# Kernel optimization log

Measured on AMD Instinct MI355X. Metric: run time of the kernel, lower is better.

## Reference

```python
import jax, jax.numpy as jnp
import numpy as np

T, B, E, H = 64, 64, 128, 256
N_ITEMS, N_DATA = 50000, 20000
EPS = 1e-8


def setup_inputs() -> dict:
    key = jax.random.key(0)
    ks = jax.random.split(key, 20)
    lengths = jnp.sort(jax.random.randint(ks[0], (B,), 1, T + 1))[::-1]
    lengths = lengths.at[0].set(T)  # pack_padded_sequence expects max length first
    x = jax.random.randint(ks[1], (T, B), 1, N_ITEMS)
    tmask = jnp.arange(T)[:, None] < lengths[None, :]
    x = jnp.where(tmask, x, 0)  # padding index 0
    s = 0.05
    emb_table = (jax.random.normal(ks[2], (N_ITEMS, E)) * s).at[0].set(0.0)  # padding_idx=0
    data_embeddings = jax.random.normal(ks[3], (N_DATA, E)) * s
    return {
        'x': x, 'lengths': lengths,
        'emb_table': emb_table, 'data_embeddings': data_embeddings,
        'W_ih': jax.random.normal(ks[4], (4 * H, E)) * s,
        'W_hh': jax.random.normal(ks[5], (4 * H, H)) * s,
        'b_ih': jax.random.normal(ks[6], (4 * H,)) * s,
        'b_hh': jax.random.normal(ks[7], (4 * H,)) * s,
        'Wq': jax.random.normal(ks[8], (H, H)) * s, 'bq': jax.random.normal(ks[9], (H,)) * s,
        'Wk': jax.random.normal(ks[10], (H, H)) * s, 'bk': jax.random.normal(ks[11], (H,)) * s,
        'Wv': jax.random.normal(ks[12], (H, H)) * s, 'bv': jax.random.normal(ks[13], (H,)) * s,
        'W_out': jax.random.normal(ks[14], (E, H)) * s, 'b_out': jax.random.normal(ks[15], (E,)) * s,
    }


def _forward(x, lengths, emb_table, data_embeddings, W_ih, W_hh, b_ih, b_hh,
             Wq, bq, Wk, bk, Wv, bv, W_out, b_out):
    t_len, b_sz = x.shape
    e_dim = emb_table.shape[1]
    h_dim = W_hh.shape[1]

    embs0 = emb_table[x]  # (T, B, E); dropout is identity in eval mode
    initial_embs = jax.lax.stop_gradient(embs0)  # .clone().detach() in original

    # PositionalEncoding: original slices by x.size(1) == batch dim (faithful quirk)
    pos = jnp.arange(b_sz, dtype=jnp.float32)[:, None]
    div = jnp.exp(jnp.arange(0, e_dim, 2, dtype=jnp.float32) * (-jnp.log(10000.0) / e_dim))
    enc = jnp.stack([jnp.sin(pos * div), jnp.cos(pos * div)], axis=-1).reshape(b_sz, e_dim)
    embs = embs0 + enc[None, :, :]  # broadcast over time

    # single-layer LSTM over time (gate order i, f, g, o)
    def step(carry, x_t):
        h, c = carry
        gates = x_t @ W_ih.T + h @ W_hh.T + (b_ih + b_hh)  # (B, 4H)
        i, f, g, o = jnp.split(gates, 4, axis=-1)
        c = jax.nn.sigmoid(f) * c + jax.nn.sigmoid(i) * jnp.tanh(g)
        h = jax.nn.sigmoid(o) * jnp.tanh(c)
        return (h, c), h

    h0 = jnp.zeros((b_sz, h_dim), embs.dtype)
    (_, _), lstm_out = jax.lax.scan(step, (h0, h0), embs)  # (T, B, H)

    # pack/pad round-trip zeroes outputs past each length (LSTM is causal)
    tmask = jnp.arange(t_len)[:, None] < lengths[None, :]  # (T, B)
    lstm_out = lstm_out * tmask[:, :, None]
    lstm_out = lstm_out.transpose(1, 0, 2)  # (B, T, H)

    padding_mask = jnp.sum(lstm_out, axis=-1) != 0  # (B, T)

    q = lstm_out @ Wq.T + bq
    k = lstm_out @ Wk.T + bk
    v = lstm_out @ Wv.T + bv
    score = jnp.einsum('bth,bsh->bts', q, k) / jnp.sqrt(jnp.float32(h_dim))
    score = jnp.where(padding_mask[:, None, :], score, -jnp.inf)
    attn = jax.nn.softmax(score, axis=2)
    weighted = jnp.einsum('bts,bsh->bth', attn, v)  # (B, T, H)
    attn_output = jnp.mean(weighted, axis=1) @ W_out.T + b_out  # (B, E)

    # kNN: fused normalize + matmul + argmin + gather over all T at once
    qn = initial_embs / jnp.clip(jnp.linalg.norm(initial_embs, axis=-1, keepdims=True), EPS)
    dn = data_embeddings / jnp.clip(jnp.linalg.norm(data_embeddings, axis=-1, keepdims=True), EPS)
    sims = jnp.einsum('tbe,ne->tbn', qn, dn)  # (T, B, N_DATA)
    idx = jnp.argmax(sims, axis=-1)  # argmin of (1 - sim)
    closest = jnp.mean(data_embeddings[idx], axis=0)  # (B, E)

    attn_output = attn_output * closest
    return attn_output @ emb_table.T  # (B, n_items)


def reference(x, lengths, emb_table, data_embeddings, W_ih, W_hh, b_ih, b_hh,
              Wq, bq, Wk, bk, Wv, bv, W_out, b_out):
    return _forward(x, lengths, emb_table, data_embeddings, W_ih, W_hh, b_ih, b_hh,
                    Wq, bq, Wk, bk, Wv, bv, W_out, b_out)
```

## Files before the change

kernel.cpp:

```cpp
#include <hip/hip_runtime.h>

typedef unsigned int uint;
typedef unsigned short ushort;
typedef unsigned long long u64;

#define NITEMS 50000
#define NDATA  20000
#define BLKCAP 4096u
#define OVCAP  65536u

#define OFF_LSTMOUT   0x0000000ULL
#define OFF_HX        0x0400000ULL
#define OFF_HXM       0x0440000ULL
#define OFF_PACKED    0x0480000ULL
#define OFF_PACKED2   0x0488000ULL
#define OFF_HITCNTS   0x0490000ULL
#define OFF_OHITCNT   0x0490800ULL
#define MEMSET_BYTES  0x0491000ULL
#define OFF_QMARGIN   0x0491000ULL
#define OFF_XW        0x05A0000ULL
#define OFF_QKV       0x15A0000ULL
#define OFF_HITBUF    OFF_QKV
#define OFF_WIHT      0x21A0000ULL
#define OFF_WQKVT     0x2220000ULL
#define OFF_BIASIH    0x22E0000ULL
#define OFF_BQKV      0x22E1000ULL
#define OFF_DNSCALE   0x22E2000ULL
#define OFF_CLOSEST   0x22F6000ULL
#define OFF_AV        0x22FE000ULL
#define OFF_DEMB16    0x2306000ULL
#define OFF_A16       0x27E8000ULL

__device__ __forceinline__ ushort f2bf(float f) {
  union { float f; uint u; } v; v.f = f;
  uint u = v.u;
  return (ushort)((u + 0x7FFFu + ((u >> 16) & 1u)) >> 16);
}
__device__ __forceinline__ uint fkey(float f) {
  union { float f; uint u; } v; v.f = f;
  return (v.u & 0x80000000u) ? ~v.u : (v.u | 0x80000000u);
}
__device__ __forceinline__ u64 shfl_xor_u64(u64 v, int off) {
  uint lo = (uint)v, hi = (uint)(v >> 32);
  lo = (uint)__shfl_xor((int)lo, off);
  hi = (uint)__shfl_xor((int)hi, off);
  return ((u64)hi << 32) | (u64)lo;
}

typedef __attribute__((ext_vector_type(8))) short short8;
typedef __attribute__((ext_vector_type(4))) float floatx4;

#define R32(M) M(0) M(1) M(2) M(3) M(4) M(5) M(6) M(7) M(8) M(9) M(10) M(11) \
  M(12) M(13) M(14) M(15) M(16) M(17) M(18) M(19) M(20) M(21) M(22) M(23) \
  M(24) M(25) M(26) M(27) M(28) M(29) M(30) M(31)

__global__ __launch_bounds__(256) void prep_kernel(
    const int* __restrict__ x,
    const float* __restrict__ emb, const float* __restrict__ demb,
    const float* __restrict__ W_ih,
    const float* __restrict__ Wq, const float* __restrict__ Wk, const float* __restrict__ Wv,
    const float* __restrict__ b_ih, const float* __restrict__ b_hh,
    const float* __restrict__ bq, const float* __restrict__ bk, const float* __restrict__ bv,
    float* __restrict__ dnscale, ushort* __restrict__ demb16, ushort* __restrict__ a16,
    float* __restrict__ wiht, float* __restrict__ wqkvt,
    float* __restrict__ biasih, float* __restrict__ bqkv,
    float* __restrict__ qmargin, u64* __restrict__ packed2)
{
  int blk = blockIdx.x, tid = threadIdx.x;
  if (blk < 5000) {
    int row = blk * 4 + (tid >> 6);
    int lane = tid & 63;
    float2 d = *(const float2*)(demb + (size_t)row * 128 + lane * 2);
    float s = d.x * d.x + d.y * d.y;
    for (int off = 32; off; off >>= 1) s += __shfl_xor(s, off);
    if (lane == 0) dnscale[row] = 1.0f / fmaxf(sqrtf(s), 1e-8f);
  } else if (blk < 6250) {
    size_t base = ((size_t)(blk - 5000) * 256 + tid) * 8;
    float4 f1 = *(const float4*)(demb + base);
    float4 f2 = *(const float4*)(demb + base + 4);
    uint4 o;
    o.x = (uint)f2bf(f1.x) | ((uint)f2bf(f1.y) << 16);
    o.y = (uint)f2bf(f1.z) | ((uint)f2bf(f1.w) << 16);
    o.z = (uint)f2bf(f2.x) | ((uint)f2bf(f2.y) << 16);
    o.w = (uint)f2bf(f2.z) | ((uint)f2bf(f2.w) << 16);
    *(uint4*)(demb16 + base) = o;
  } else if (blk < 6506) {
    int idx = (blk - 6250) * 256 + tid;
    int m = idx >> 4, seg = idx & 15;
    const float* src = emb + (size_t)x[m] * 128 + seg * 8;
    float4 f1 = *(const float4*)(src);
    float4 f2 = *(const float4*)(src + 4);
    uint4 o;
    o.x = (uint)f2bf(f1.x) | ((uint)f2bf(f1.y) << 16);
    o.y = (uint)f2bf(f1.z) | ((uint)f2bf(f1.w) << 16);
    o.z = (uint)f2bf(f2.x) | ((uint)f2bf(f2.y) << 16);
    o.w = (uint)f2bf(f2.z) | ((uint)f2bf(f2.w) << 16);
    *(uint4*)(a16 + (size_t)m * 128 + seg * 8) = o;
  } else if (blk < 7018) {
    int f = (blk - 6506) * 256 + tid;
    int r = f >> 7, e = f & 127;
    wiht[e * 1024 + r] = W_ih[f];
  } else if (blk < 7786) {
    int f = (blk - 7018) * 256 + tid;
    int w = f >> 16; int rem = f & 65535;
    int r = rem >> 8, e = rem & 255;
    const float* src = (w == 0) ? Wq : (w == 1) ? Wk : Wv;
    wqkvt[e * 768 + w * 256 + r] = src[rem];
  } else if (blk < 7790) {
    int idx = (blk - 7786) * 256 + tid;
    if (idx < 1024) biasih[idx] = b_ih[idx] + b_hh[idx];
  } else if (blk < 7793) {
    int idx = (blk - 7790) * 256 + tid;
    if (idx < 768) {
      int w = idx >> 8; int r = idx & 255;
      const float* src = (w == 0) ? bq : (w == 1) ? bk : bv;
      bqkv[idx] = src[r];
    }
  } else {
    int row = (blk - 7793) * 4 + (tid >> 6);
    int lane = tid & 63;
    float2 d = *(const float2*)(emb + (size_t)x[row] * 128 + lane * 2);
    float s = d.x * d.x + d.y * d.y;
    for (int off = 32; off; off >>= 1) s += __shfl_xor(s, off);
    if (lane == 0) {
      if (s == 0.f) {
        qmargin[row] = -1e30f;
        packed2[row] = ((u64)fkey(0.0f) << 32) | 0xFFFFFFFFull;
      } else {
        qmargin[row] = 0.017f * sqrtf(s) + 1e-5f;
      }
    }
  }
}

__global__ __launch_bounds__(256) void xw_kernel(
    const int* __restrict__ x, const float* __restrict__ emb,
    const float* __restrict__ wiht, const float* __restrict__ biasih,
    float* __restrict__ xW)
{
  __shared__ __align__(16) float At[128 * 16];
  int blk = blockIdx.x, tid = threadIdx.x;
  int m0 = blk * 16;
  for (int c = 0; c < 8; ++c) {
    int idx = c * 256 + tid;
    int mm = idx >> 7, e = idx & 127;
    int m = m0 + mm;
    int bcol = m & 63;
    int xv = x[m];
    float val = emb[(size_t)xv * 128 + e];
    int j = e >> 1;
    float arg = (float)bcol * __expf((float)j * -0.14391157f);
    val += (e & 1) ? cosf(arg) : sinf(arg);
    At[e * 16 + mm] = val;
  }
  __syncthreads();
  int quad = tid >> 6, l = tid & 63;
  for (int rp = 0; rp < 4; ++rp) {
    int r = rp * 256 + l * 4;
    float acc[4][4] = {};
    for (int e = 0; e < 128; ++e) {
      float4 wv4 = *(const float4*)(wiht + e * 1024 + r);
      float4 av4 = *(const float4*)(At + e * 16 + quad * 4);
      float am[4] = {av4.x, av4.y, av4.z, av4.w};
      float wr4[4] = {wv4.x, wv4.y, wv4.z, wv4.w};
      #pragma unroll
      for (int mi = 0; mi < 4; ++mi)
        #pragma unroll
        for (int ri = 0; ri < 4; ++ri)
          acc[mi][ri] += am[mi] * wr4[ri];
    }
    float4 bv4 = *(const float4*)(biasih + r);
    #pragma unroll
    for (int mi = 0; mi < 4; ++mi) {
      size_t m = (size_t)(m0 + quad * 4 + mi);
      float4 o;
      o.x = acc[mi][0] + bv4.x; o.y = acc[mi][1] + bv4.y;
      o.z = acc[mi][2] + bv4.z; o.w = acc[mi][3] + bv4.w;
      *(float4*)(xW + m * 1024 + r) = o;
    }
  }
}

__global__ __launch_bounds__(256) void knn_kernel(
    const ushort* __restrict__ a16, const ushort* __restrict__ demb16,
    const float* __restrict__ dnscale, const float* __restrict__ qmargin,
    u64* __restrict__ packed, uint* __restrict__ hitcnts, uint* __restrict__ ohitcnt,
    uint* __restrict__ hitbuf)
{
  __shared__ __align__(16) ushort b_sh[2][64 * 144];
  __shared__ uint lcnt;
  int blk = blockIdx.x, tid = threadIdx.x;
  int chunk = blk & 15, mt = blk >> 4;
  int wv = tid >> 6, lane = tid & 63;
  int col = lane & 15, quad = lane >> 4;
  int M0 = mt * 128;
  if (tid == 0) lcnt = 0;
  short8 afrag[2][4];
  #pragma unroll
  for (int s = 0; s < 2; ++s) {
    int mrow = M0 + s * 64 + wv * 16 + col;
    #pragma unroll
    for (int kf = 0; kf < 4; ++kf)
      afrag[s][kf] = *(const short8*)(a16 + (size_t)mrow * 128 + kf * 32 + quad * 8);
  }
  float best[2][4] = {{-1e30f,-1e30f,-1e30f,-1e30f},{-1e30f,-1e30f,-1e30f,-1e30f}};
  int bidx[2][4] = {};
  int nbase = chunk * 1250, nend = nbase + 1250;
  const int niter = 20;
  int srow = tid >> 4, sseg = tid & 15;
  uint4 stg[4]; float scr[4];

  #pragma unroll
  for (int p = 0; p < 4; ++p) {
    int n = nbase + p * 16 + srow;
    uint4 v = {0u,0u,0u,0u};
    if (n < nend) v = *(const uint4*)(demb16 + (size_t)n * 128 + sseg * 8);
    stg[p] = v;
  }
  #pragma unroll
  for (int ns = 0; ns < 4; ++ns) {
    int n = nbase + ns * 16 + col;
    scr[ns] = (n < nend) ? dnscale[n] : 0.f;
  }
  for (int it = 0; it < niter; ++it) {
    int n0 = nbase + it * 64;
    ushort* bsh = b_sh[it & 1];
    #pragma unroll
    for (int p = 0; p < 4; ++p)
      *(uint4*)(&bsh[(p * 16 + srow) * 144 + sseg * 8]) = stg[p];
    float mysc[4] = {scr[0], scr[1], scr[2], scr[3]};
    __syncthreads();
    if (it + 1 < niter) {
      int nb = n0 + 64;
      #pragma unroll
      for (int p = 0; p < 4; ++p) {
        int n = nb + p * 16 + srow;
        uint4 v = {0u,0u,0u,0u};
        if (n < nend) v = *(const uint4*)(demb16 + (size_t)n * 128 + sseg * 8);
        stg[p] = v;
      }
      #pragma unroll
      for (int ns = 0; ns < 4; ++ns) {
        int n = nb + ns * 16 + col;
        scr[ns] = (n < nend) ? dnscale[n] : 0.f;
      }
    }
    #pragma unroll
    for (int ns = 0; ns < 4; ++ns) {
      short8 bfr[4];
      #pragma unroll
      for (int kf = 0; kf < 4; ++kf)
        bfr[kf] = *(const short8*)(&bsh[(ns * 16 + col) * 144 + kf * 32 + quad * 8]);
      int n = n0 + ns * 16 + col;
      float sc = mysc[ns];
      bool valid = (n < nend);
      #pragma unroll
      for (int s = 0; s < 2; ++s) {
        floatx4 acc = {0.f, 0.f, 0.f, 0.f};
        #pragma unroll
        for (int kf = 0; kf < 4; ++kf)
          acc = __builtin_amdgcn_mfma_f32_16x16x32_bf16(afrag[s][kf], bfr[kf], acc, 0, 0, 0);
        #pragma unroll
        for (int r = 0; r < 4; ++r) {
          float sim = acc[r] * sc;
          if (valid && sim > best[s][r]) { best[s][r] = sim; bidx[s][r] = n; }
        }
      }
    }
  }
  float thr[2][4];
  #pragma unroll
  for (int s = 0; s < 2; ++s)
    #pragma unroll
    for (int r = 0; r < 4; ++r) {
      u64 p = ((u64)fkey(best[s][r]) << 32) | (u64)(0xFFFFFFFFu - (uint)bidx[s][r]);
      #pragma unroll
      for (int off = 1; off < 16; off <<= 1) {
        u64 o = shfl_xor_u64(p, off);
        if (o > p) p = o;
      }
      int m = M0 + s * 64 + wv * 16 + quad * 4 + r;
      union { uint u; float f; } bu;
      uint k = (uint)(p >> 32);
      bu.u = (k & 0x80000000u) ? (k & 0x7FFFFFFFu) : ~k;
      thr[s][r] = bu.f - qmargin[m];
      if (col == 0)
        atomicMax((unsigned long long*)&packed[m], (unsigned long long)p);
    }
  __syncthreads();

  uint* myregion = hitbuf + (size_t)blk * BLKCAP;
  uint* ovregion = hitbuf + (size_t)512 * BLKCAP;
  #pragma unroll
  for (int p = 0; p < 4; ++p) {
    int n = nbase + p * 16 + srow;
    uint4 v = {0u,0u,0u,0u};
    if (n < nend) v = *(const uint4*)(demb16 + (size_t)n * 128 + sseg * 8);
    stg[p] = v;
  }
  #pragma unroll
  for (int ns = 0; ns < 4; ++ns) {
    int n = nbase + ns * 16 + col;
    scr[ns] = (n < nend) ? dnscale[n] : 0.f;
  }
  for (int it = 0; it < niter; ++it) {
    int n0 = nbase + it * 64;
    ushort* bsh = b_sh[it & 1];
    #pragma unroll
    for (int p = 0; p < 4; ++p)
      *(uint4*)(&bsh[(p * 16 + srow) * 144 + sseg * 8]) = stg[p];
    float mysc[4] = {scr[0], scr[1], scr[2], scr[3]};
    __syncthreads();
    if (it + 1 < niter) {
      int nb = n0 + 64;
      #pragma unroll
      for (int p = 0; p < 4; ++p) {
        int n = nb + p * 16 + srow;
        uint4 v = {0u,0u,0u,0u};
        if (n < nend) v = *(const uint4*)(demb16 + (size_t)n * 128 + sseg * 8);
        stg[p] = v;
      }
      #pragma unroll
      for (int ns = 0; ns < 4; ++ns) {
        int n = nb + ns * 16 + col;
        scr[ns] = (n < nend) ? dnscale[n] : 0.f;
      }
    }
    #pragma unroll
    for (int ns = 0; ns < 4; ++ns) {
      short8 bfr[4];
      #pragma unroll
      for (int kf = 0; kf < 4; ++kf)
        bfr[kf] = *(const short8*)(&bsh[(ns * 16 + col) * 144 + kf * 32 + quad * 8]);
      int n = n0 + ns * 16 + col;
      float sc = mysc[ns];
      bool valid = (n < nend);
      #pragma unroll
      for (int s = 0; s < 2; ++s) {
        floatx4 acc = {0.f, 0.f, 0.f, 0.f};
        #pragma unroll
        for (int kf = 0; kf < 4; ++kf)
          acc = __builtin_amdgcn_mfma_f32_16x16x32_bf16(afrag[s][kf], bfr[kf], acc, 0, 0, 0);
        #pragma unroll
        for (int r = 0; r < 4; ++r) {
          float sim = acc[r] * sc;
          bool hit = valid && (sim >= thr[s][r]);
          u64 mask = __ballot(hit);
          if (mask) {
            uint lcntv = (uint)__popcll(mask);
            int leader = __ffsll((unsigned long long)mask) - 1;
            uint base = 0;
            if (lane == leader) base = atomicAdd(&lcnt, lcntv);
            base = (uint)__shfl((int)base, leader);
            if (hit) {
              uint pos = base + (uint)__popcll(mask & ((1ull << lane) - 1ull));
              uint mm = (uint)(M0 + s * 64 + wv * 16 + quad * 4 + r);
              uint rec = (mm << 15) | (uint)n;
              if (pos < BLKCAP) {
                myregion[pos] = rec;
              } else {
                uint op = atomicAdd(ohitcnt, 1u);
                if (op < OVCAP) ovregion[op] = rec;
              }
            }
          }
        }
      }
    }
  }
  __syncthreads();
  if (tid == 0) hitcnts[blk] = lcnt;
}

__global__ __launch_bounds__(256) void rescore_kernel(
    const uint* __restrict__ hitbuf, const uint* __restrict__ hitcnts,
    const uint* __restrict__ ohitcnt, const u64* __restrict__ packed,
    const int* __restrict__ x, const float* __restrict__ emb,
    const float* __restrict__ demb, const float* __restrict__ dnscale,
    u64* __restrict__ packed2)
{
  int blk = blockIdx.x, tid = threadIdx.x;
  uint gid = blk * 256 + tid;
  if (gid < 4096) {
    uint m = gid;
    uint n = 0xFFFFFFFFu - (uint)(packed[m] & 0xFFFFFFFFull);
    if (n < NDATA) {
      const float* q = emb + (size_t)x[m] * 128;
      const float* d = demb + (size_t)n * 128;
      double p = 0.0;
      #pragma unroll 8
      for (int e = 0; e < 128; e += 2) {
        float2 qv = *(const float2*)(q + e);
        float2 dv = *(const float2*)(d + e);
        p += (double)qv.x * (double)dv.x + (double)qv.y * (double)dv.y;
      }
      float sx = (float)(p * (double)dnscale[n]);
      u64 key = ((u64)fkey(sx) << 32) | (u64)(0xFFFFFFFFu - n);
      atomicMax((unsigned long long*)&packed2[m], (unsigned long long)key);
    }
  }
  const uint* src; uint cnt; uint stride;
  if (blk < 512) {
    src = hitbuf + (size_t)blk * BLKCAP;
    cnt = hitcnts[blk]; if (cnt > BLKCAP) cnt = BLKCAP;
    stride = 256;
  } else {
    src = hitbuf + (size_t)512 * BLKCAP;
    cnt = *ohitcnt; if (cnt > OVCAP) cnt = OVCAP;
    stride = 16 * 256;
  }
  uint start = (blk < 512) ? tid : (uint)((blk - 512) * 256 + tid);
  for (uint h = start; h < cnt; h += stride) {
    uint rec = src[h];
    uint m = rec >> 15, n = rec & 0x7FFFu;
    if (m >= 4096 || n >= NDATA) continue;
    const float* q = emb + (size_t)x[m] * 128;
    const float* d = demb + (size_t)n * 128;
    double p = 0.0;
    #pragma unroll 8
    for (int e = 0; e < 128; e += 2) {
      float2 qv = *(const float2*)(q + e);
      float2 dv = *(const float2*)(d + e);
      p += (double)qv.x * (double)dv.x + (double)qv.y * (double)dv.y;
    }
    float sx = (float)(p * (double)dnscale[n]);
    u64 key = ((u64)fkey(sx) << 32) | (u64)(0xFFFFFFFFu - n);
    atomicMax((unsigned long long*)&packed2[m], (unsigned long long)key);
  }
}

__global__ __launch_bounds__(512, 2) void lstm_kernel(
    const int* __restrict__ lengths, const float* __restrict__ Whh,
    const float* __restrict__ xW, float* __restrict__ lstm_out,
    u64* __restrict__ hx, u64* __restrict__ hxm)
{
  __shared__ __align__(16) float h_sh[256];
  __shared__ float part_sh[256];
  int blk = blockIdx.x, tid = threadIdx.x;
  int b = blk & 63, q = blk >> 6;
  int row_local = tid >> 1, half = tid & 1;
  int gate = row_local >> 6, jloc = row_local & 63;
  int grow = gate * 256 + q * 64 + jloc;
  const float4* wp4 = (const float4*)(Whh + (size_t)grow * 256 + half * 128);
#define WDECL(i) float4 tt##i = wp4[i]; \
  float w##i##x = tt##i.x, w##i##y = tt##i.y, w##i##z = tt##i.z, w##i##w = tt##i.w;
  R32(WDECL)
#define WPIN(i) asm volatile("" : "+v"(w##i##x), "+v"(w##i##y), "+v"(w##i##z), "+v"(w##i##w));
  R32(WPIN)
  int len = lengths[b];
  if (tid < 256) h_sh[tid] = 0.f;
  float cval = 0.f;
  int prm = tid - 320;
  int jr = (prm < q * 64) ? prm : prm + 64;
  bool fast_ok = true;
  __syncthreads();
  for (int t = 0; t < len; ++t) {
    float xw0, xw1, xw2, xw3;
    if (tid < 64) {
      const float* xwrow = xW + ((size_t)t * 64 + b) * 1024 + q * 64 + tid;
      xw0 = xwrow[0]; xw1 = xwrow[256]; xw2 = xwrow[512]; xw3 = xwrow[768];
    }
    const float4* h4 = (const float4*)(h_sh + half * 128);
    float acc = 0.f;
#define WACC(i) { float4 hv = h4[i]; \
    acc += w##i##x * hv.x + w##i##y * hv.y + w##i##z * hv.z + w##i##w * hv.w; }
    R32(WACC)
    acc += __shfl_xor(acc, 1);
    if (!half) part_sh[row_local] = acc;
    __syncthreads();
    if (tid < 64) {
      float gi = part_sh[tid]       + xw0;
      float gf = part_sh[64 + tid]  + xw1;
      float gg = part_sh[128 + tid] + xw2;
      float go = part_sh[192 + tid] + xw3;
      float ii = 1.f / (1.f + __expf(-gi));
      float ff = 1.f / (1.f + __expf(-gf));
      float oo = 1.f / (1.f + __expf(-go));
      float tg = 1.f - 2.f / (1.f + __expf(2.f * gg));
      cval = ff * cval + ii * tg;
      float tc = 1.f - 2.f / (1.f + __expf(2.f * cval));
      float hv = oo * tc;
      int j = q * 64 + tid;
      union { float f; uint u; } cu; cu.f = hv;
      u64 pk = ((u64)cu.u << 32) | (u64)(uint)(t + 1);
      size_t slot = ((size_t)((t + 1) & 1) * 64 + b) * 256 + j;
      asm volatile("global_store_dwordx2 %0, %1, off"
                   :: "v"(hxm + slot), "v"(pk) : "memory");
      __hip_atomic_store(hx + slot, pk, __ATOMIC_RELAXED, __HIP_MEMORY_SCOPE_AGENT);
      h_sh[j] = hv;
      lstm_out[((size_t)b * 64 + t) * 256 + j] = hv;
    } else if (tid >= 320 && t + 1 < len) {
      size_t slot = ((size_t)((t + 1) & 1) * 64 + b) * 256 + jr;
      uint want = (uint)(t + 1);
      u64 v = 0;
      bool got = false;
      if (fast_ok) {
        const u64* ms = hxm + slot;
        for (int tries = 0; tries < 32; ++tries) {
          asm volatile("global_load_dwordx2 %0, %1, off sc0\n\t"
                       "s_waitcnt vmcnt(0)"
                       : "=&v"(v) : "v"(ms) : "memory");
          if ((uint)v == want) { got = true; break; }
        }
        if (!got && t > 0) fast_ok = false;
      }
      if (!got) {
        const u64* as = hx + slot;
        int guard = 0;
        while (true) {
          v = __hip_atomic_load(as, __ATOMIC_RELAXED, __HIP_MEMORY_SCOPE_AGENT);
          if ((uint)v == want || ++guard > (1 << 22)) break;
        }
      }
      union { uint u; float f; } cv; cv.u = (uint)(v >> 32);
      h_sh[jr] = cv.f;
    }
    __syncthreads();
  }
}

__global__ __launch_bounds__(128) void closest_kernel(
    const u64* __restrict__ packed2, const float* __restrict__ demb,
    float* __restrict__ closest)
{
  int b = blockIdx.x, tid = threadIdx.x;
  float s = 0.f;
  for (int t = 0; t < 64; ++t) {
    uint low = (uint)(packed2[t * 64 + b] & 0xFFFFFFFFull);
    uint n = 0xFFFFFFFFu - low;
    if (n >= NDATA) n = 0;
    s += demb[(size_t)n * 128 + tid];
  }
  closest[b * 128 + tid] = s * (1.0f / 64.0f);
}

__global__ __launch_bounds__(256) void qkv_kernel(
    const float* __restrict__ lstm_out, const float* __restrict__ wqkvt,
    const float* __restrict__ bqkv, float* __restrict__ qkv)
{
  __shared__ __align__(16) float At[256 * 16];
  int blk = blockIdx.x, tid = threadIdx.x;
  int m0 = blk * 16;
  for (int c = 0; c < 16; ++c)
    At[tid * 16 + c] = lstm_out[((size_t)m0 + c) * 256 + tid];
  __syncthreads();
  int quad = tid >> 6, l = tid & 63;
  for (int rp = 0; rp < 3; ++rp) {
    int r = rp * 256 + l * 4;
    float acc[4][4] = {};
    for (int e = 0; e < 256; ++e) {
      float4 wv4 = *(const float4*)(wqkvt + (size_t)e * 768 + r);
      float4 av4 = *(const float4*)(At + e * 16 + quad * 4);
      float am[4] = {av4.x, av4.y, av4.z, av4.w};
      float wr4[4] = {wv4.x, wv4.y, wv4.z, wv4.w};
      #pragma unroll
      for (int mi = 0; mi < 4; ++mi)
        #pragma unroll
        for (int ri = 0; ri < 4; ++ri)
          acc[mi][ri] += am[mi] * wr4[ri];
    }
    float4 bv4 = *(const float4*)(bqkv + r);
    #pragma unroll
    for (int mi = 0; mi < 4; ++mi) {
      size_t m = (size_t)(m0 + quad * 4 + mi);
      float4 o;
      o.x = acc[mi][0] + bv4.x; o.y = acc[mi][1] + bv4.y;
      o.z = acc[mi][2] + bv4.z; o.w = acc[mi][3] + bv4.w;
      *(float4*)(qkv + m * 768 + r) = o;
    }
  }
}

__global__ __launch_bounds__(256) void attn_kernel(
    const float* __restrict__ qkv, const int* __restrict__ lengths,
    const float* __restrict__ closest, const float* __restrict__ W_out,
    const float* __restrict__ b_out, float* __restrict__ av)
{
  __shared__ float k_sh[64 * 257];
  __shared__ __align__(16) float q_sh[4 * 256];
  __shared__ float wpart[4 * 64];
  __shared__ float wtot[64];
  __shared__ float out_sh[256];
  int b = blockIdx.x, tid = threadIdx.x;
  int wv = tid >> 6, lane = tid & 63;
  int len = lengths[b];
  for (int s = 0; s < 64; ++s)
    k_sh[s * 257 + tid] = qkv[((size_t)b * 64 + s) * 768 + 256 + tid];
  wpart[tid] = 0.f;
  for (int tq = 0; tq < 16; ++tq) {
    __syncthreads();
    #pragma unroll
    for (int c = 0; c < 4; ++c)
      q_sh[c * 256 + tid] = qkv[((size_t)b * 64 + tq * 4 + c) * 768 + tid];
    __syncthreads();
    const float* krow = k_sh + lane * 257;
    const float* qrow = q_sh + wv * 256;
    float sc = 0.f;
    #pragma unroll 8
    for (int h = 0; h < 256; ++h)
      sc += qrow[h] * krow[h];
    sc *= 0.0625f;
    bool vs = (lane < len);
    float scm = vs ? sc : -1e30f;
    float mx = scm;
    for (int off = 32; off; off >>= 1) mx = fmaxf(mx, __shfl_xor(mx, off));
    float e = vs ? __expf(sc - mx) : 0.f;
    float sum = e;
    for (int off = 32; off; off >>= 1) sum += __shfl_xor(sum, off);
    wpart[wv * 64 + lane] += e / sum;
  }
  __syncthreads();
  if (tid < 64)
    wtot[tid] = (wpart[tid] + wpart[64 + tid] + wpart[128 + tid] + wpart[192 + tid]) * (1.0f / 64.0f);
  __syncthreads();
  {
    float acc = 0.f;
    for (int s = 0; s < 64; ++s)
      acc += wtot[s] * qkv[((size_t)b * 64 + s) * 768 + 512 + tid];
    out_sh[tid] = acc;
  }
  __syncthreads();
  if (tid < 128) {
    const float4* wr = (const float4*)(W_out + (size_t)tid * 256);
    float p = b_out[tid];
    #pragma unroll
    for (int c = 0; c < 64; ++c) {
      float4 u = wr[c];
      p += out_sh[c * 4 + 0] * u.x + out_sh[c * 4 + 1] * u.y
         + out_sh[c * 4 + 2] * u.z + out_sh[c * 4 + 3] * u.w;
    }
    av[tid * 64 + b] = p * closest[b * 128 + tid];
  }
}

__global__ __launch_bounds__(256) void final_kernel(
    const float* __restrict__ emb, const float* __restrict__ av,
    float* __restrict__ out)
{
  int i = blockIdx.x * 256 + threadIdx.x;
  if (i >= NITEMS) return;
  const float4* row = (const float4*)(emb + (size_t)i * 128);
  float acc[64];
  #pragma unroll
  for (int bb = 0; bb < 64; ++bb) acc[bb] = 0.f;
  for (int e4 = 0; e4 < 32; ++e4) {
    float4 u = row[e4];
    float wvv[4] = {u.x, u.y, u.z, u.w};
    const float* ab = av + e4 * 4 * 64;
    #pragma unroll
    for (int j = 0; j < 4; ++j) {
      #pragma unroll
      for (int bb = 0; bb < 64; ++bb)
        acc[bb] += wvv[j] * ab[j * 64 + bb];
    }
  }
  #pragma unroll
  for (int bb = 0; bb < 64; ++bb)
    out[(size_t)bb * NITEMS + i] = acc[bb];
}

extern "C" void kernel_launch(void* const* d_in, const int* in_sizes, int n_in,
                              void* d_out, int out_size, void* d_ws, size_t ws_size,
                              hipStream_t stream)
{
  const int*   x       = (const int*)d_in[0];
  const int*   lengths = (const int*)d_in[1];
  const float* emb     = (const float*)d_in[2];
  const float* demb    = (const float*)d_in[3];
  const float* W_ih    = (const float*)d_in[4];
  const float* W_hh    = (const float*)d_in[5];
  const float* b_ih    = (const float*)d_in[6];
  const float* b_hh    = (const float*)d_in[7];
  const float* Wq      = (const float*)d_in[8];
  const float* bq      = (const float*)d_in[9];
  const float* Wk      = (const float*)d_in[10];
  const float* bk      = (const float*)d_in[11];
  const float* Wv      = (const float*)d_in[12];
  const float* bv      = (const float*)d_in[13];
  const float* W_out   = (const float*)d_in[14];
  const float* b_out   = (const float*)d_in[15];

  char* ws = (char*)d_ws;
  float*  lstm_out = (float*)(ws + OFF_LSTMOUT);
  u64*    hx       = (u64*)(ws + OFF_HX);
  u64*    hxm      = (u64*)(ws + OFF_HXM);
  u64*    packed   = (u64*)(ws + OFF_PACKED);
  u64*    packed2  = (u64*)(ws + OFF_PACKED2);
  uint*   hitcnts  = (uint*)(ws + OFF_HITCNTS);
  uint*   ohitcnt  = (uint*)(ws + OFF_OHITCNT);
  float*  qmargin  = (float*)(ws + OFF_QMARGIN);
  uint*   hitbuf   = (uint*)(ws + OFF_HITBUF);
  float*  xW       = (float*)(ws + OFF_XW);
  float*  qkv      = (float*)(ws + OFF_QKV);
  float*  wiht     = (float*)(ws + OFF_WIHT);
  float*  wqkvt    = (float*)(ws + OFF_WQKVT);
  float*  biasih   = (float*)(ws + OFF_BIASIH);
  float*  bqkv     = (float*)(ws + OFF_BQKV);
  float*  dnscale  = (float*)(ws + OFF_DNSCALE);
  float*  closest  = (float*)(ws + OFF_CLOSEST);
  float*  av       = (float*)(ws + OFF_AV);
  ushort* demb16   = (ushort*)(ws + OFF_DEMB16);
  ushort* a16      = (ushort*)(ws + OFF_A16);

  hipMemsetAsync(d_ws, 0, (size_t)MEMSET_BYTES, stream);

  hipLaunchKernelGGL(prep_kernel, dim3(8817), dim3(256), 0, stream,
                     x, emb, demb, W_ih, Wq, Wk, Wv, b_ih, b_hh, bq, bk, bv,
                     dnscale, demb16, a16, wiht, wqkvt, biasih, bqkv,
                     qmargin, packed2);
  hipLaunchKernelGGL(xw_kernel, dim3(256), dim3(256), 0, stream,
                     x, emb, wiht, biasih, xW);
  hipLaunchKernelGGL(knn_kernel, dim3(512), dim3(256), 0, stream,
                     a16, demb16, dnscale, qmargin, packed, hitcnts, ohitcnt, hitbuf);
  hipLaunchKernelGGL(rescore_kernel, dim3(528), dim3(256), 0, stream,
                     hitbuf, hitcnts, ohitcnt, packed, x, emb, demb, dnscale, packed2);
  hipLaunchKernelGGL(lstm_kernel, dim3(256), dim3(512), 0, stream,
                     lengths, W_hh, xW, lstm_out, hx, hxm);
  hipLaunchKernelGGL(closest_kernel, dim3(64), dim3(128), 0, stream,
                     packed2, demb, closest);
  hipLaunchKernelGGL(qkv_kernel, dim3(256), dim3(256), 0, stream,
                     lstm_out, wqkvt, bqkv, qkv);
  hipLaunchKernelGGL(attn_kernel, dim3(64), dim3(256), 0, stream,
                     qkv, lengths, closest, W_out, b_out, av);
  hipLaunchKernelGGL(final_kernel, dim3(196), dim3(256), 0, stream,
                     emb, av, (float*)d_out);
}
```

Baseline: 609.7 us.

## Prefetch next-step xW, offload lstm_out stores, pad h_sh, use lighter barriers in LSTM

Result: no change. 599.5 us (-1.7%).

```diff
diff --git a/kernel.cpp b/kernel.cpp
--- a/kernel.cpp
+++ b/kernel.cpp
@@ -53,6 +53,15 @@
 #define R32(M) M(0) M(1) M(2) M(3) M(4) M(5) M(6) M(7) M(8) M(9) M(10) M(11) \
   M(12) M(13) M(14) M(15) M(16) M(17) M(18) M(19) M(20) M(21) M(22) M(23) \
   M(24) M(25) M(26) M(27) M(28) M(29) M(30) M(31)
+
+#define HIX(j) ((j) + (((j) >> 7) << 2))
+
+#define LBAR() do { \
+  __builtin_amdgcn_sched_barrier(0); \
+  asm volatile("s_waitcnt lgkmcnt(0)" ::: "memory"); \
+  __builtin_amdgcn_s_barrier(); \
+  __builtin_amdgcn_sched_barrier(0); \
+} while (0)
 
 __global__ __launch_bounds__(256) void prep_kernel(
     const int* __restrict__ x,
@@ -434,7 +443,7 @@
     const float* __restrict__ xW, float* __restrict__ lstm_out,
     u64* __restrict__ hx, u64* __restrict__ hxm)
 {
-  __shared__ __align__(16) float h_sh[256];
+  __shared__ __align__(16) float h_sh[264];
   __shared__ float part_sh[256];
   int blk = blockIdx.x, tid = threadIdx.x;
   int b = blk & 63, q = blk >> 6;
@@ -448,26 +457,35 @@
 #define WPIN(i) asm volatile("" : "+v"(w##i##x), "+v"(w##i##y), "+v"(w##i##z), "+v"(w##i##w));
   R32(WPIN)
   int len = lengths[b];
-  if (tid < 256) h_sh[tid] = 0.f;
+  if (tid < 256) h_sh[HIX(tid)] = 0.f;
   float cval = 0.f;
   int prm = tid - 320;
   int jr = (prm < q * 64) ? prm : prm + 64;
   bool fast_ok = true;
+  int j1 = q * 64 + (tid - 64);
+  float xw0 = 0.f, xw1 = 0.f, xw2 = 0.f, xw3 = 0.f;
+  if (tid < 64) {
+    const float* xwrow = xW + ((size_t)0 * 64 + b) * 1024 + q * 64 + tid;
+    xw0 = xwrow[0]; xw1 = xwrow[256]; xw2 = xwrow[512]; xw3 = xwrow[768];
+  }
   __syncthreads();
   for (int t = 0; t < len; ++t) {
-    float xw0, xw1, xw2, xw3;
-    if (tid < 64) {
-      const float* xwrow = xW + ((size_t)t * 64 + b) * 1024 + q * 64 + tid;
-      xw0 = xwrow[0]; xw1 = xwrow[256]; xw2 = xwrow[512]; xw3 = xwrow[768];
-    }
-    const float4* h4 = (const float4*)(h_sh + half * 128);
-    float acc = 0.f;
-#define WACC(i) { float4 hv = h4[i]; \
-    acc += w##i##x * hv.x + w##i##y * hv.y + w##i##z * hv.z + w##i##w * hv.w; }
+    float nx0 = 0.f, nx1 = 0.f, nx2 = 0.f, nx3 = 0.f;
+    if (tid < 64 && t + 1 < len) {
+      const float* xwrow = xW + ((size_t)(t + 1) * 64 + b) * 1024 + q * 64 + tid;
+      nx0 = xwrow[0]; nx1 = xwrow[256]; nx2 = xwrow[512]; nx3 = xwrow[768];
+    }
+    float hprev = 0.f;
+    if (tid >= 64 && tid < 128 && t > 0) hprev = h_sh[HIX(j1)];
+    const float4* h4 = (const float4*)(h_sh + half * 132);
+    float a[4] = {0.f, 0.f, 0.f, 0.f};
+#define WACC(i) { float4 hv_ = h4[i]; \
+    a[(i) & 3] += w##i##x * hv_.x + w##i##y * hv_.y + w##i##z * hv_.z + w##i##w * hv_.w; }
     R32(WACC)
+    float acc = (a[0] + a[2]) + (a[1] + a[3]);
     acc += __shfl_xor(acc, 1);
     if (!half) part_sh[row_local] = acc;
-    __syncthreads();
+    LBAR();
     if (tid < 64) {
       float gi = part_sh[tid]       + xw0;
       float gf = part_sh[64 + tid]  + xw1;
@@ -484,11 +502,15 @@
       union { float f; uint u; } cu; cu.f = hv;
       u64 pk = ((u64)cu.u << 32) | (u64)(uint)(t + 1);
       size_t slot = ((size_t)((t + 1) & 1) * 64 + b) * 256 + j;
+      __builtin_amdgcn_sched_barrier(0);
+      asm volatile("s_waitcnt vmcnt(4)" ::: "memory");
       asm volatile("global_store_dwordx2 %0, %1, off"
                    :: "v"(hxm + slot), "v"(pk) : "memory");
       __hip_atomic_store(hx + slot, pk, __ATOMIC_RELAXED, __HIP_MEMORY_SCOPE_AGENT);
-      h_sh[j] = hv;
-      lstm_out[((size_t)b * 64 + t) * 256 + j] = hv;
+      h_sh[HIX(j)] = hv;
+      xw0 = nx0; xw1 = nx1; xw2 = nx2; xw3 = nx3;
+    } else if (tid < 128) {
+      if (t > 0) lstm_out[((size_t)b * 64 + (t - 1)) * 256 + j1] = hprev;
     } else if (tid >= 320 && t + 1 < len) {
       size_t slot = ((size_t)((t + 1) & 1) * 64 + b) * 256 + jr;
       uint want = (uint)(t + 1);
@@ -509,13 +531,17 @@
         int guard = 0;
         while (true) {
           v = __hip_atomic_load(as, __ATOMIC_RELAXED, __HIP_MEMORY_SCOPE_AGENT);
-          if ((uint)v == want || ++guard > (1 << 22)) break;
+          if ((uint)v == want || ++guard > (1 << 24)) break;
         }
       }
       union { uint u; float f; } cv; cv.u = (uint)(v >> 32);
-      h_sh[jr] = cv.f;
-    }
-    __syncthreads();
+      h_sh[HIX(jr)] = cv.f;
+    }
+    LBAR();
+  }
+  if (tid >= 64 && tid < 128) {
+    float hl = h_sh[HIX(j1)];
+    lstm_out[((size_t)b * 64 + (len - 1)) * 256 + j1] = hl;
   }
 }
 
```
